# Kernel optimization log

Hardware: AMD Instinct MI355X
Metric: run time of the kernel (lower is better)

Reference implementation:

```python
import jax, jax.numpy as jnp
from jax import lax
import numpy as np

N, C, D, KNN = 32768, 1000, 1024, 16
EPS_EUC = 1e-12
EPS_COS = 1e-8
COS_THRESH = 0.85


def setup_inputs() -> dict:
    key = jax.random.key(0)
    k1, k2, k3 = jax.random.split(key, 3)
    feature = jax.random.normal(k1, (N, D), dtype=jnp.float32)
    pred = jax.random.normal(k2, (N, C), dtype=jnp.float32)
    unlabeled_index = jnp.arange(N, dtype=jnp.int64) if jax.config.jax_enable_x64 else jnp.arange(N, dtype=jnp.int32)
    # module state: centroids (from FeaturePool), top-N score buffer (init -1), fake index buffer (init -1)
    centroids = jax.random.normal(k3, (C, D), dtype=jnp.float32)
    pred_top_N = jnp.full((C, KNN), -1.0, dtype=jnp.float32)
    fake_index = jnp.full((C, KNN), -1, dtype=jnp.int32)
    return {"feature": feature, "pred": pred, "unlabeled_index": unlabeled_index,
            "centroids": centroids, "pred_top_N": pred_top_N, "fake_index": fake_index}


def reference(feature, pred, unlabeled_index, centroids, pred_top_N, fake_index):
    xx = jnp.sum(feature * feature, axis=1, keepdims=True)          # [N,1]
    yy = jnp.sum(centroids * centroids, axis=1)[None, :]            # [1,C]
    euc = jnp.sqrt(jnp.clip(xx + yy - 2.0 * (feature @ centroids.T), EPS_EUC, None))
    euc_id = jnp.argmin(euc, axis=1)                                # [N]

    scores = jnp.max(jax.nn.softmax(pred, axis=1), axis=1)          # [N] max softmax prob

    # cosine similarity of every sample to every centroid [N, C]
    f_n = feature / jnp.clip(jnp.linalg.norm(feature, axis=1, keepdims=True), EPS_COS, None)
    c_n = centroids / jnp.clip(jnp.linalg.norm(centroids, axis=1, keepdims=True), EPS_COS, None)
    cos = f_n @ c_n.T
    label_idx = jnp.argmax(cos, axis=1)                             # [N]
    cos_max = jnp.max(cos, axis=1)                                  # [N]

    # label[i] = label_idx if (cos-argmax == euc-argmin and cos_max > 0.85) else -1
    label = jnp.where((label_idx == euc_id) & (cos_max > COS_THRESH),
                      label_idx.astype(jnp.float32), -1.0)

    # sequential bounded top-N scatter update of (pred_top_N, fake_index)
    def step(carry, x):
        ptn, fidx = carry
        li, sc, ui = x
        row = ptn[li]                        # [KNN]
        mi = jnp.argmin(row)
        upd = sc > row[mi]
        ptn = ptn.at[li, mi].set(jnp.where(upd, sc, row[mi]))
        fidx = fidx.at[li, mi].set(jnp.where(upd, ui.astype(fidx.dtype), fidx[li, mi]))
        return (ptn, fidx), None

    (ptn_new, fidx_new), _ = lax.scan(step, (pred_top_N, fake_index),
                                      (label_idx, scores, unlabeled_index))
    return label, ptn_new, fidx_new
```

## Files before the change

### kernel.cpp

```cpp
#include <hip/hip_runtime.h>
#include <hip/hip_bf16.h>
#include <math.h>

#define NS 32768
#define NC 1000
#define CP 1024
#define DD 1024
#define KN 16

typedef __attribute__((ext_vector_type(8))) short bf16x8;
typedef __attribute__((ext_vector_type(4))) float f32x4;
typedef __attribute__((ext_vector_type(4))) float float4v;
typedef __attribute__((ext_vector_type(4))) int int4v;
typedef __attribute__((ext_vector_type(8))) unsigned short u16x8;
typedef __attribute__((ext_vector_type(4))) unsigned short u16x4;

__device__ __forceinline__ unsigned short f2bf(float f) {
  unsigned u = __float_as_uint(f);
  u += 0x7FFFu + ((u >> 16) & 1u);
  return (unsigned short)(u >> 16);
}
__device__ __forceinline__ float bf2f(unsigned short h) {
  return __uint_as_float(((unsigned)h) << 16);
}

#define GLL16(g, l) __builtin_amdgcn_global_load_lds( \
    (const __attribute__((address_space(1))) void*)(g), \
    (__attribute__((address_space(3))) void*)(l), 16, 0, 0)

#define PREP_FEAT_BLKS (NS * DD / 8 / 256)
__global__ __launch_bounds__(256) void k_prep(
    const float* __restrict__ Cm, unsigned short* __restrict__ Cb,
    float* __restrict__ cnorm2, float* __restrict__ invc,
    const float* __restrict__ A, unsigned short* __restrict__ Ab,
    const float* __restrict__ P, float* __restrict__ scores) {
  __shared__ float red[4];
  __shared__ float wmax[4];
  __shared__ double wsum[4];
  int b = blockIdx.x, tid = threadIdx.x;
  int lane = tid & 63, wid = tid >> 6;
  if (b < NS) {
    const float* row = P + (size_t)b * NC;
    bool act = tid < 250;
    float p0 = 0, p1 = 0, p2 = 0, p3 = 0, mx = -1e30f;
    if (act) {
      int o = tid * 4;
      p0 = row[o]; p1 = row[o + 1]; p2 = row[o + 2]; p3 = row[o + 3];
      mx = fmaxf(fmaxf(p0, p1), fmaxf(p2, p3));
    }
    for (int off = 32; off; off >>= 1) mx = fmaxf(mx, __shfl_xor(mx, off));
    if (!lane) wmax[wid] = mx;
    __syncthreads();
    float m = fmaxf(fmaxf(wmax[0], wmax[1]), fmaxf(wmax[2], wmax[3]));
    double s = 0.0;
    if (act)
      s = (double)__expf(p0 - m) + (double)__expf(p1 - m) +
          (double)__expf(p2 - m) + (double)__expf(p3 - m);
    for (int off = 32; off; off >>= 1) s += __shfl_xor(s, off);
    if (!lane) wsum[wid] = s;
    __syncthreads();
    if (!tid) scores[b] = (float)(1.0 / (wsum[0] + wsum[1] + wsum[2] + wsum[3]));
  } else if (b < NS + PREP_FEAT_BLKS) {
    int t = (b - NS) * 256 + tid;
    const float4v* src = (const float4v*)A + (size_t)t * 2;
    float4v a = src[0], v = src[1];
    u16x8 o = { f2bf(a[0]), f2bf(a[1]), f2bf(a[2]), f2bf(a[3]),
                f2bf(v[0]), f2bf(v[1]), f2bf(v[2]), f2bf(v[3]) };
    *(u16x8*)(Ab + (size_t)t * 8) = o;
  } else {
    int c = b - NS - PREP_FEAT_BLKS;
    float sq = 0.f;
    if (c < NC) {
      float4v v = ((const float4v*)(Cm + (size_t)c * DD))[tid];
      sq = v[0]*v[0] + v[1]*v[1] + v[2]*v[2] + v[3]*v[3];
      u16x4 o = { f2bf(v[0]), f2bf(v[1]), f2bf(v[2]), f2bf(v[3]) };
      *(u16x4*)(Cb + (size_t)c * DD + tid * 4) = o;
    } else {
      u16x4 z = { 0, 0, 0, 0 };
      *(u16x4*)(Cb + (size_t)c * DD + tid * 4) = z;
    }
    for (int off = 32; off; off >>= 1) sq += __shfl_xor(sq, off);
    if (!lane) red[wid] = sq;
    __syncthreads();
    if (!tid) {
      float s = red[0] + red[1] + red[2] + red[3];
      cnorm2[c] = s;
      float n = sqrtf(s); if (n < 1e-8f) n = 1e-8f;
      invc[c] = (c < NC) ? 1.0f / n : 0.0f;
    }
  }
}

#define MF(a_, b_, c_) __builtin_amdgcn_mfma_f32_16x16x32_bf16(a_, b_, c_, 0, 0, 0)
#define RD(base_, i_) (*(const bf16x8*)((base_) + (i_) * 1024 + aoff))
#define SA(s_, b_) do { \
    GLL16(pA0 + (s_) * 32, ldsB + (b_) * 16384 + dA0); \
    GLL16(pA1 + (s_) * 32, ldsB + (b_) * 16384 + dA1); } while (0)
#define SB(s_, b_) do { \
    GLL16(pB0 + (s_) * 32, ldsB + 65536 + (b_) * 16384 + dA0); \
    GLL16(pB1 + (s_) * 32, ldsB + 65536 + (b_) * 16384 + dA1); } while (0)
#define VM4 asm volatile("s_waitcnt vmcnt(4)" ::: "memory")
#define VM0 asm volatile("s_waitcnt vmcnt(0)" ::: "memory")
#define MFMAC(A0_, A1_, A2_, A3_, M0) do { \
    acc[M0+0][0] = MF(A0_, bv0, acc[M0+0][0]); \
    acc[M0+0][1] = MF(A0_, bv1, acc[M0+0][1]); \
    acc[M0+0][2] = MF(A0_, bv2, acc[M0+0][2]); \
    acc[M0+0][3] = MF(A0_, bv3, acc[M0+0][3]); \
    acc[M0+1][0] = MF(A1_, bv0, acc[M0+1][0]); \
    acc[M0+1][1] = MF(A1_, bv1, acc[M0+1][1]); \
    acc[M0+1][2] = MF(A1_, bv2, acc[M0+1][2]); \
    acc[M0+1][3] = MF(A1_, bv3, acc[M0+1][3]); \
    acc[M0+2][0] = MF(A2_, bv0, acc[M0+2][0]); \
    acc[M0+2][1] = MF(A2_, bv1, acc[M0+2][1]); \
    acc[M0+2][2] = MF(A2_, bv2, acc[M0+2][2]); \
    acc[M0+2][3] = MF(A2_, bv3, acc[M0+2][3]); \
    acc[M0+3][0] = MF(A3_, bv0, acc[M0+3][0]); \
    acc[M0+3][1] = MF(A3_, bv1, acc[M0+3][1]); \
    acc[M0+3][2] = MF(A3_, bv2, acc[M0+3][2]); \
    acc[M0+3][3] = MF(A3_, bv3, acc[M0+3][3]); } while (0)
#define KSTEP(s_, STAGE_, GATE_) do { \
    const char* Ab_ = ldsB + ((s_) & 3) * 16384 + wrOff; \
    const char* Bb_ = ldsB + 65536 + ((s_) & 3) * 16384 + wcOff; \
    af0 = RD(Ab_, 0); af1 = RD(Ab_, 1); af2 = RD(Ab_, 2); af3 = RD(Ab_, 3); \
    bv0 = RD(Bb_, 0); bv1 = RD(Bb_, 1); bv2 = RD(Bb_, 2); bv3 = RD(Bb_, 3); \
    af4 = RD(Ab_, 4); af5 = RD(Ab_, 5); af6 = RD(Ab_, 6); af7 = RD(Ab_, 7); \
    STAGE_; \
    __builtin_amdgcn_s_setprio(1); \
    MFMAC(af0, af1, af2, af3, 0); \
    MFMAC(af4, af5, af6, af7, 4); \
    __builtin_amdgcn_s_setprio(0); \
    GATE_; \
    __builtin_amdgcn_s_barrier(); \
  } while (0)

__global__ __launch_bounds__(512, 1) void k_gemm(
    const unsigned short* __restrict__ A,
    const unsigned short* __restrict__ B,
    unsigned short* __restrict__ Dout) {
  __shared__ unsigned short lds[65536];
  char* ldsB = (char*)lds;
  int tid = threadIdx.x, lane = tid & 63, wid = tid >> 6;
  int wr = wid >> 2, wc = wid & 3;
  int bid = (blockIdx.x & 7) * 64 + (blockIdx.x >> 3);
  int cb = bid & 3, rb = bid >> 2;
  int brow = rb * 256, bcol = cb * 256;

  f32x4 acc[8][4];
#pragma unroll
  for (int m = 0; m < 8; ++m)
#pragma unroll
    for (int n = 0; n < 4; ++n) acc[m][n] = (f32x4){0.f, 0.f, 0.f, 0.f};

  int f0 = wid * 64 + lane, f1 = f0 + 512;
  int gl0 = (f0 & 3) ^ ((f0 >> 3) & 3);
  int gl1 = (f1 & 3) ^ ((f1 >> 3) & 3);
  const unsigned short* pA0 = A + (size_t)(brow + (f0 >> 2)) * DD + gl0 * 8;
  const unsigned short* pA1 = A + (size_t)(brow + (f1 >> 2)) * DD + gl1 * 8;
  const unsigned short* pB0 = B + (size_t)(bcol + (f0 >> 2)) * DD + gl0 * 8;
  const unsigned short* pB1 = B + (size_t)(bcol + (f1 >> 2)) * DD + gl1 * 8;
  int dA0 = f0 * 16, dA1 = f1 * 16;

  int aoff = (lane & 15) * 64 + (((lane >> 4) ^ ((lane >> 1) & 3)) * 16);
  int wrOff = wr * 8192;
  int wcOff = wc * 4096;

  bf16x8 af0, af1, af2, af3, af4, af5, af6, af7, bv0, bv1, bv2, bv3;

  SA(0, 0); SB(0, 0);
  SA(1, 1); SB(1, 1);
  VM4;
  __builtin_amdgcn_s_barrier();

  for (int s = 0; s < 30; ++s) {
    int bn = (s + 2) & 3;
    KSTEP(s, { SA(s + 2, bn); SB(s + 2, bn); }, VM4);
  }
  KSTEP(30, (void)0, VM0);
  KSTEP(31, (void)0, (void)0);

  int colb = bcol + wc * 64 + (lane & 15);
  int rowb = brow + wr * 128 + ((lane >> 4) << 2);
#pragma unroll
  for (int m = 0; m < 8; ++m)
#pragma unroll
    for (int n = 0; n < 4; ++n)
#pragma unroll
      for (int j = 0; j < 4; ++j)
        Dout[(size_t)(rowb + m * 16 + j) * CP + colb + n * 16] = f2bf(acc[m][n][j]);
}

__global__ __launch_bounds__(256) void k_argmax(
    const unsigned short* __restrict__ Dot, const float* __restrict__ invc,
    const float* __restrict__ cnorm2, const float* __restrict__ feat,
    const float* __restrict__ cent, float* __restrict__ label_out,
    int* __restrict__ lidx) {
  __shared__ float s_inv[CP], s_cn[CP];
  int tid = threadIdx.x;
#pragma unroll
  for (int q = 0; q < 4; ++q) {
    int c = q * 256 + tid;
    s_inv[c] = invc[c]; s_cn[c] = cnorm2[c];
  }
  __syncthreads();
  int lane = tid & 63, wid = tid >> 6;
  int i = blockIdx.x * 4 + wid;
  const unsigned short* drow = Dot + (size_t)i * CP;

  float v[16];
  float dmax = -1e30f; int darg = CP;
  float emin = 1e30f;  int earg = CP;
#pragma unroll
  for (int it = 0; it < 16; ++it) {
    int c = it * 64 + lane;
    float val, ev;
    if (c < NC) {
      float d = bf2f(drow[c]);
      val = d * s_inv[c];
      ev = s_cn[c] - 2.0f * d;
    } else { val = -1e30f; ev = 1e30f; }
    v[it] = val;
    if (val > dmax) { dmax = val; darg = c; }
    if (ev < emin)  { emin = ev;  earg = c; }
  }
  for (int off = 32; off; off >>= 1) {
    float om = __shfl_xor(dmax, off); int oi = __shfl_xor(darg, off);
    if (om > dmax || (om == dmax && oi < darg)) { dmax = om; darg = oi; }
    float oe = __shfl_xor(emin, off); int oj = __shfl_xor(earg, off);
    if (oe < emin || (oe == emin && oj < earg)) { emin = oe; earg = oj; }
  }
  const float MARGIN = 0.15f;
  unsigned long long cmask[16]; int ccnt = 0;
#pragma unroll
  for (int it = 0; it < 16; ++it) {
    int c = it * 64 + lane;
    bool cand = (c < NC) && (v[it] >= dmax - MARGIN);
    cmask[it] = __ballot(cand);
    ccnt += __popcll(cmask[it]);
  }
  int finalArg = darg;
  double cosmax_d = -2.0;
  bool need = (ccnt > 1) || (dmax > 10.0f);
  if (need) {
    float xv[16]; double sx = 0.0;
    const float* xr = feat + (size_t)i * DD;
#pragma unroll
    for (int t = 0; t < 16; ++t) {
      float x = xr[t * 64 + lane]; xv[t] = x; sx += (double)x * (double)x;
    }
    for (int off = 32; off; off >>= 1) sx += __shfl_xor(sx, off);
    double nx = sqrt(sx); if (nx < 1e-8) nx = 1e-8;
    double best = -2.0; int besti = CP;
    for (int it = 0; it < 16; ++it) {
      unsigned long long mk = cmask[it];
      while (mk) {
        int b = __builtin_ctzll(mk); mk &= mk - 1;
        int c = it * 64 + b;
        const float* cr = cent + (size_t)c * DD;
        double s = 0.0, s2 = 0.0;
#pragma unroll
        for (int t = 0; t < 16; ++t) {
          double cv = (double)cr[t * 64 + lane];
          s += (double)xv[t] * cv; s2 += cv * cv;
        }
        for (int off = 32; off; off >>= 1) {
          s += __shfl_xor(s, off); s2 += __shfl_xor(s2, off);
        }
        double nc = sqrt(s2); if (nc < 1e-8) nc = 1e-8;
        double cs = s / (nx * nc);
        if (cs > best) { best = cs; besti = c; }
      }
    }
    finalArg = besti; cosmax_d = best;
  }
  if (!lane) {
    lidx[i] = finalArg;
    float lab = -1.0f;
    if (need && finalArg == earg && cosmax_d > 0.85) lab = (float)finalArg;
    label_out[i] = lab;
  }
}

__global__ __launch_bounds__(64) void k_scan(
    const int* __restrict__ lidx, const float* __restrict__ scores,
    const int* __restrict__ uidx, const float* __restrict__ ptn_in,
    const int* __restrict__ fidx_in, float* __restrict__ out_ptn,
    float* __restrict__ out_fidx) {
  int c = blockIdx.x;
  int lane = threadIdx.x;
  float row[KN]; int idx[KN];
#pragma unroll
  for (int j = 0; j < KN; ++j) {
    row[j] = ptn_in[c * KN + j];
    idx[j] = fidx_in[c * KN + j];
  }
  for (int base = 0; base < NS; base += 256) {
    int l0 = lidx[base + lane];
    int l1 = lidx[base + 64 + lane];
    int l2 = lidx[base + 128 + lane];
    int l3 = lidx[base + 192 + lane];
#pragma unroll
    for (int q = 0; q < 4; ++q) {
      int lab = (q == 0) ? l0 : (q == 1) ? l1 : (q == 2) ? l2 : l3;
      unsigned long long m = __ballot(lab == c);
      while (m) {
        int b = __builtin_ctzll(m); m &= m - 1;
        int i = base + q * 64 + b;
        float s = scores[i];
        int ui = uidx[i];
        int mi = 0; float mn = row[0];
#pragma unroll
        for (int t = 1; t < KN; ++t)
          if (row[t] < mn) { mn = row[t]; mi = t; }
        if (s > mn) {
#pragma unroll
          for (int t = 0; t < KN; ++t)
            if (t == mi) { row[t] = s; idx[t] = ui; }
        }
      }
    }
  }
  if (!lane) {
#pragma unroll
    for (int j = 0; j < KN; ++j) {
      out_ptn[c * KN + j] = row[j];
      out_fidx[c * KN + j] = (float)idx[j];
    }
  }
}

extern "C" void kernel_launch(void* const* d_in, const int* in_sizes, int n_in,
                              void* d_out, int out_size, void* d_ws, size_t ws_size,
                              hipStream_t stream) {
  const float* feature = (const float*)d_in[0];
  const float* pred    = (const float*)d_in[1];
  const int*   uidx    = (const int*)d_in[2];
  const float* cent    = (const float*)d_in[3];
  const float* ptn_in  = (const float*)d_in[4];
  const int*   fidx_in = (const int*)d_in[5];
  float* out = (float*)d_out;

  char* ws = (char*)d_ws;
  unsigned short* cent_bf = (unsigned short*)(ws);
  unsigned short* feat_bf = (unsigned short*)(ws + (2ull << 20));
  unsigned short* dot_bf  = (unsigned short*)(ws + (66ull << 20));
  float* scores = (float*)(ws + (130ull << 20));
  int*   lidx   = (int*)  (ws + (130ull << 20) + (128ull << 10));
  float* cnorm2 = (float*)(ws + (130ull << 20) + (256ull << 10));
  float* invc   = (float*)(ws + (130ull << 20) + (260ull << 10));

  hipLaunchKernelGGL(k_prep, dim3(NS + PREP_FEAT_BLKS + CP), dim3(256), 0, stream,
                     cent, cent_bf, cnorm2, invc,
                     feature, feat_bf, pred, scores);
  hipLaunchKernelGGL(k_gemm, dim3((NS / 256) * (CP / 256)), dim3(512), 0, stream,
                     feat_bf, cent_bf, dot_bf);
  hipLaunchKernelGGL(k_argmax, dim3(NS / 4), dim3(256), 0, stream,
                     dot_bf, invc, cnorm2, feature, cent, out, lidx);
  hipLaunchKernelGGL(k_scan, dim3(NC), dim3(64), 0, stream,
                     lidx, scores, uidx, ptn_in, fidx_in,
                     out + NS, out + NS + NC * KN);
}
```

Measured before the change: 224.5 us.

## Fuse softmax max-probability into GEMM kernel using extra specialized waves

The per-row max-softmax score computation moves out of the prep kernel and into the GEMM kernel. Four extra waves per 768-thread block each handle 16 rows of pred, while the original eight waves do the MFMA tile. The score waves match the GEMM waves' barrier count so the two groups run in lockstep. The aim is to hide the large pred read behind the compute-bound GEMM. The cost is a lower per-wave register budget under the larger launch bound, which risks spilling the GEMM accumulators, plus memory bandwidth contention with the GEMM loads.

```diff
diff --git a/kernel.cpp b/kernel.cpp
--- a/kernel.cpp
+++ b/kernel.cpp
@@ -32,43 +32,19 @@
 __global__ __launch_bounds__(256) void k_prep(
     const float* __restrict__ Cm, unsigned short* __restrict__ Cb,
     float* __restrict__ cnorm2, float* __restrict__ invc,
-    const float* __restrict__ A, unsigned short* __restrict__ Ab,
-    const float* __restrict__ P, float* __restrict__ scores) {
+    const float* __restrict__ A, unsigned short* __restrict__ Ab) {
   __shared__ float red[4];
-  __shared__ float wmax[4];
-  __shared__ double wsum[4];
   int b = blockIdx.x, tid = threadIdx.x;
   int lane = tid & 63, wid = tid >> 6;
-  if (b < NS) {
-    const float* row = P + (size_t)b * NC;
-    bool act = tid < 250;
-    float p0 = 0, p1 = 0, p2 = 0, p3 = 0, mx = -1e30f;
-    if (act) {
-      int o = tid * 4;
-      p0 = row[o]; p1 = row[o + 1]; p2 = row[o + 2]; p3 = row[o + 3];
-      mx = fmaxf(fmaxf(p0, p1), fmaxf(p2, p3));
-    }
-    for (int off = 32; off; off >>= 1) mx = fmaxf(mx, __shfl_xor(mx, off));
-    if (!lane) wmax[wid] = mx;
-    __syncthreads();
-    float m = fmaxf(fmaxf(wmax[0], wmax[1]), fmaxf(wmax[2], wmax[3]));
-    double s = 0.0;
-    if (act)
-      s = (double)__expf(p0 - m) + (double)__expf(p1 - m) +
-          (double)__expf(p2 - m) + (double)__expf(p3 - m);
-    for (int off = 32; off; off >>= 1) s += __shfl_xor(s, off);
-    if (!lane) wsum[wid] = s;
-    __syncthreads();
-    if (!tid) scores[b] = (float)(1.0 / (wsum[0] + wsum[1] + wsum[2] + wsum[3]));
-  } else if (b < NS + PREP_FEAT_BLKS) {
-    int t = (b - NS) * 256 + tid;
-    const float4v* src = (const float4v*)A + (size_t)t * 2;
+  if (b < PREP_FEAT_BLKS) {
+    size_t t = (size_t)b * 256 + tid;
+    const float4v* src = (const float4v*)A + t * 2;
     float4v a = src[0], v = src[1];
     u16x8 o = { f2bf(a[0]), f2bf(a[1]), f2bf(a[2]), f2bf(a[3]),
                 f2bf(v[0]), f2bf(v[1]), f2bf(v[2]), f2bf(v[3]) };
-    *(u16x8*)(Ab + (size_t)t * 8) = o;
+    *(u16x8*)(Ab + t * 8) = o;
   } else {
-    int c = b - NS - PREP_FEAT_BLKS;
+    int c = b - PREP_FEAT_BLKS;
     float sq = 0.f;
     if (c < NC) {
       float4v v = ((const float4v*)(Cm + (size_t)c * DD))[tid];
@@ -133,60 +109,98 @@
     __builtin_amdgcn_s_barrier(); \
   } while (0)
 
-__global__ __launch_bounds__(512, 1) void k_gemm(
+__global__ __launch_bounds__(768, 1) void k_gemm(
     const unsigned short* __restrict__ A,
     const unsigned short* __restrict__ B,
-    unsigned short* __restrict__ Dout) {
+    unsigned short* __restrict__ Dout,
+    const float* __restrict__ P,
+    float* __restrict__ scores) {
   __shared__ unsigned short lds[65536];
   char* ldsB = (char*)lds;
   int tid = threadIdx.x, lane = tid & 63, wid = tid >> 6;
-  int wr = wid >> 2, wc = wid & 3;
-  int bid = (blockIdx.x & 7) * 64 + (blockIdx.x >> 3);
-  int cb = bid & 3, rb = bid >> 2;
-  int brow = rb * 256, bcol = cb * 256;
-
-  f32x4 acc[8][4];
-#pragma unroll
-  for (int m = 0; m < 8; ++m)
-#pragma unroll
-    for (int n = 0; n < 4; ++n) acc[m][n] = (f32x4){0.f, 0.f, 0.f, 0.f};
-
-  int f0 = wid * 64 + lane, f1 = f0 + 512;
-  int gl0 = (f0 & 3) ^ ((f0 >> 3) & 3);
-  int gl1 = (f1 & 3) ^ ((f1 >> 3) & 3);
-  const unsigned short* pA0 = A + (size_t)(brow + (f0 >> 2)) * DD + gl0 * 8;
-  const unsigned short* pA1 = A + (size_t)(brow + (f1 >> 2)) * DD + gl1 * 8;
-  const unsigned short* pB0 = B + (size_t)(bcol + (f0 >> 2)) * DD + gl0 * 8;
-  const unsigned short* pB1 = B + (size_t)(bcol + (f1 >> 2)) * DD + gl1 * 8;
-  int dA0 = f0 * 16, dA1 = f1 * 16;
-
-  int aoff = (lane & 15) * 64 + (((lane >> 4) ^ ((lane >> 1) & 3)) * 16);
-  int wrOff = wr * 8192;
-  int wcOff = wc * 4096;
-
-  bf16x8 af0, af1, af2, af3, af4, af5, af6, af7, bv0, bv1, bv2, bv3;
-
-  SA(0, 0); SB(0, 0);
-  SA(1, 1); SB(1, 1);
-  VM4;
-  __builtin_amdgcn_s_barrier();
-
-  for (int s = 0; s < 30; ++s) {
-    int bn = (s + 2) & 3;
-    KSTEP(s, { SA(s + 2, bn); SB(s + 2, bn); }, VM4);
-  }
-  KSTEP(30, (void)0, VM0);
-  KSTEP(31, (void)0, (void)0);
-
-  int colb = bcol + wc * 64 + (lane & 15);
-  int rowb = brow + wr * 128 + ((lane >> 4) << 2);
-#pragma unroll
-  for (int m = 0; m < 8; ++m)
-#pragma unroll
-    for (int n = 0; n < 4; ++n)
-#pragma unroll
-      for (int j = 0; j < 4; ++j)
-        Dout[(size_t)(rowb + m * 16 + j) * CP + colb + n * 16] = f2bf(acc[m][n][j]);
+
+  if (wid < 8) {
+    int wr = wid >> 2, wc = wid & 3;
+    int bid = (blockIdx.x & 7) * 64 + (blockIdx.x >> 3);
+    int cb = bid & 3, rb = bid >> 2;
+    int brow = rb * 256, bcol = cb * 256;
+
+    f32x4 acc[8][4];
+#pragma unroll
+    for (int m = 0; m < 8; ++m)
+#pragma unroll
+      for (int n = 0; n < 4; ++n) acc[m][n] = (f32x4){0.f, 0.f, 0.f, 0.f};
+
+    int f0 = wid * 64 + lane, f1 = f0 + 512;
+    int gl0 = (f0 & 3) ^ ((f0 >> 3) & 3);
+    int gl1 = (f1 & 3) ^ ((f1 >> 3) & 3);
+    const unsigned short* pA0 = A + (size_t)(brow + (f0 >> 2)) * DD + gl0 * 8;
+    const unsigned short* pA1 = A + (size_t)(brow + (f1 >> 2)) * DD + gl1 * 8;
+    const unsigned short* pB0 = B + (size_t)(bcol + (f0 >> 2)) * DD + gl0 * 8;
+    const unsigned short* pB1 = B + (size_t)(bcol + (f1 >> 2)) * DD + gl1 * 8;
+    int dA0 = f0 * 16, dA1 = f1 * 16;
+
+    int aoff = (lane & 15) * 64 + (((lane >> 4) ^ ((lane >> 1) & 3)) * 16);
+    int wrOff = wr * 8192;
+    int wcOff = wc * 4096;
+
+    bf16x8 af0, af1, af2, af3, af4, af5, af6, af7, bv0, bv1, bv2, bv3;
+
+    SA(0, 0); SB(0, 0);
+    SA(1, 1); SB(1, 1);
+    VM4;
+    __builtin_amdgcn_s_barrier();
+
+    for (int s = 0; s < 30; ++s) {
+      int bn = (s + 2) & 3;
+      KSTEP(s, { SA(s + 2, bn); SB(s + 2, bn); }, VM4);
+    }
+    KSTEP(30, (void)0, VM0);
+    KSTEP(31, (void)0, (void)0);
+
+    int colb = bcol + wc * 64 + (lane & 15);
+    int rowb = brow + wr * 128 + ((lane >> 4) << 2);
+#pragma unroll
+    for (int m = 0; m < 8; ++m)
+#pragma unroll
+      for (int n = 0; n < 4; ++n)
+#pragma unroll
+        for (int j = 0; j < 4; ++j)
+          Dout[(size_t)(rowb + m * 16 + j) * CP + colb + n * 16] = f2bf(acc[m][n][j]);
+  } else {
+    int sw = wid - 8;
+    int rowbase = blockIdx.x * 64 + sw * 16;
+    for (int slot = 0; slot < 33; ++slot) {
+      if ((slot & 1) == 0 && slot < 32) {
+        int i = rowbase + (slot >> 1);
+        const float* row = P + (size_t)i * NC;
+        float4v p0, p1, p2, p3;
+        int col = lane * 4;
+        p0 = *(const float4v*)(row + col);
+        p1 = *(const float4v*)(row + 256 + col);
+        p2 = *(const float4v*)(row + 512 + col);
+        bool ok3 = (768 + col) < NC;
+        p3 = ok3 ? *(const float4v*)(row + 768 + col) : (float4v){0.f, 0.f, 0.f, 0.f};
+        float mx = fmaxf(fmaxf(p0[0], p0[1]), fmaxf(p0[2], p0[3]));
+        mx = fmaxf(mx, fmaxf(fmaxf(p1[0], p1[1]), fmaxf(p1[2], p1[3])));
+        mx = fmaxf(mx, fmaxf(fmaxf(p2[0], p2[1]), fmaxf(p2[2], p2[3])));
+        if (ok3) mx = fmaxf(mx, fmaxf(fmaxf(p3[0], p3[1]), fmaxf(p3[2], p3[3])));
+        for (int off = 32; off; off >>= 1) mx = fmaxf(mx, __shfl_xor(mx, off));
+        double s = (double)__expf(p0[0] - mx) + (double)__expf(p0[1] - mx) +
+                   (double)__expf(p0[2] - mx) + (double)__expf(p0[3] - mx);
+        s += (double)__expf(p1[0] - mx) + (double)__expf(p1[1] - mx) +
+             (double)__expf(p1[2] - mx) + (double)__expf(p1[3] - mx);
+        s += (double)__expf(p2[0] - mx) + (double)__expf(p2[1] - mx) +
+             (double)__expf(p2[2] - mx) + (double)__expf(p2[3] - mx);
+        if (ok3)
+          s += (double)__expf(p3[0] - mx) + (double)__expf(p3[1] - mx) +
+               (double)__expf(p3[2] - mx) + (double)__expf(p3[3] - mx);
+        for (int off = 32; off; off >>= 1) s += __shfl_xor(s, off);
+        if (!lane) scores[i] = (float)(1.0 / s);
+      }
+      __builtin_amdgcn_s_barrier();
+    }
+  }
 }
 
 __global__ __launch_bounds__(256) void k_argmax(
@@ -348,11 +362,10 @@
   float* cnorm2 = (float*)(ws + (130ull << 20) + (256ull << 10));
   float* invc   = (float*)(ws + (130ull << 20) + (260ull << 10));
 
-  hipLaunchKernelGGL(k_prep, dim3(NS + PREP_FEAT_BLKS + CP), dim3(256), 0, stream,
-                     cent, cent_bf, cnorm2, invc,
-                     feature, feat_bf, pred, scores);
-  hipLaunchKernelGGL(k_gemm, dim3((NS / 256) * (CP / 256)), dim3(512), 0, stream,
-                     feat_bf, cent_bf, dot_bf);
+  hipLaunchKernelGGL(k_prep, dim3(PREP_FEAT_BLKS + CP), dim3(256), 0, stream,
+                     cent, cent_bf, cnorm2, invc, feature, feat_bf);
+  hipLaunchKernelGGL(k_gemm, dim3((NS / 256) * (CP / 256)), dim3(768), 0, stream,
+                     feat_bf, cent_bf, dot_bf, pred, scores);
   hipLaunchKernelGGL(k_argmax, dim3(NS / 4), dim3(256), 0, stream,
                      dot_bf, invc, cnorm2, feature, cent, out, lidx);
   hipLaunchKernelGGL(k_scan, dim3(NC), dim3(64), 0, stream,
```

After: 580.3 us. 2.58x slower.
